# Performance work log

Hardware: AMD Instinct MI355X
Metric: run time of the kernel (lower is better)

## Reference

```python
import jax, jax.numpy as jnp
import numpy as np

# dipy lower-triangular channel order: [Dxx, Dxy, Dyy, Dxz, Dyz, Dzz]
_LOTRI_IDX = np.array([[0, 1, 3], [1, 2, 4], [3, 4, 5]])


def _trilinear_warp(img, ddf):
    """MONAI Warp(mode='bilinear', padding_mode='border'): sample img at voxel
    coords (index + ddf), trilinear interp, clamped to borders.
    img: (B,C,H,W,D), ddf: (B,3,H,W,D) in voxel units."""
    B, C, H, W, D = img.shape
    f = img.dtype
    gx, gy, gz = jnp.meshgrid(jnp.arange(H, dtype=f), jnp.arange(W, dtype=f),
                              jnp.arange(D, dtype=f), indexing='ij')
    cx = jnp.clip(gx[None] + ddf[:, 0], 0.0, H - 1.0)
    cy = jnp.clip(gy[None] + ddf[:, 1], 0.0, W - 1.0)
    cz = jnp.clip(gz[None] + ddf[:, 2], 0.0, D - 1.0)
    x0f = jnp.floor(cx); y0f = jnp.floor(cy); z0f = jnp.floor(cz)
    fx = (cx - x0f)[:, None]; fy = (cy - y0f)[:, None]; fz = (cz - z0f)[:, None]
    x0 = x0f.astype(jnp.int32); y0 = y0f.astype(jnp.int32); z0 = z0f.astype(jnp.int32)
    x1 = jnp.minimum(x0 + 1, H - 1); y1 = jnp.minimum(y0 + 1, W - 1); z1 = jnp.minimum(z0 + 1, D - 1)
    flat = img.reshape(B, C, H * W * D)

    def g(ix, iy, iz):
        lin = (ix * W + iy) * D + iz  # (B,H,W,D)
        return jnp.take_along_axis(flat, lin.reshape(B, 1, -1), axis=2).reshape(B, C, H, W, D)

    c00 = g(x0, y0, z0) * (1 - fz) + g(x0, y0, z1) * fz
    c01 = g(x0, y1, z0) * (1 - fz) + g(x0, y1, z1) * fz
    c10 = g(x1, y0, z0) * (1 - fz) + g(x1, y0, z1) * fz
    c11 = g(x1, y1, z0) * (1 - fz) + g(x1, y1, z1) * fz
    c0 = c00 * (1 - fy) + c01 * fy
    c1 = c10 * (1 - fy) + c11 * fy
    return c0 * (1 - fx) + c1 * fx


def _jacobian(ddf):
    """J = I + d(ddf)/dx via central differences (one-sided at edges).
    Returns (B,H,W,D,3,3) with J[...,i,j] = delta_ij + d ddf_i / d x_j."""
    rows = [jnp.stack(jnp.gradient(ddf[:, i], axis=(1, 2, 3)), axis=-1) for i in range(3)]
    J = jnp.stack(rows, axis=-2)  # (B,H,W,D,3,3)
    return J + jnp.eye(3, dtype=ddf.dtype)


def _forward(dti, ddf):
    warped = _trilinear_warp(dti, ddf)                    # (B,6,H,W,D)
    wc = jnp.moveaxis(warped, 1, -1)                      # (B,H,W,D,6)
    M = wc[..., jnp.asarray(_LOTRI_IDX)]                  # (B,H,W,D,3,3) symmetric
    J = _jacobian(ddf)
    U, _, Vh = jnp.linalg.svd(J, full_matrices=False)
    R = U @ Vh                                            # polar orthogonal factor
    Dp = jnp.einsum('...ji,...jk,...kl->...il', R, M, R)  # R^T M R
    lot = jnp.stack([Dp[..., 0, 0], Dp[..., 1, 0], Dp[..., 1, 1],
                     Dp[..., 2, 0], Dp[..., 2, 1], Dp[..., 2, 2]], axis=1)
    return lot


def setup_inputs() -> dict:
    key = jax.random.key(0)
    k1, k2 = jax.random.split(key)
    B, H, W, D = 1, 128, 128, 128
    dti = jax.random.normal(k1, (B, 6, H, W, D), dtype=jnp.float32)
    ddf = jax.random.normal(k2, (B, 3, H, W, D), dtype=jnp.float32)
    return {"dti": dti, "ddf": ddf}


def reference(dti, ddf):
    return _forward(dti, ddf)
```

## Files before the change

### kernel.cpp

```cpp
#include <hip/hip_runtime.h>
#include <hip/hip_fp16.h>
#include <math.h>

#define DIM 128
#define NVOX (DIM*DIM*DIM)

typedef float vfloat4 __attribute__((ext_vector_type(4)));
typedef unsigned int vuint4 __attribute__((ext_vector_type(4)));

__global__ __launch_bounds__(256) void pack_dti_kernel(
    const float* __restrict__ dti, vuint4* __restrict__ aos)
{
    const int bid = blockIdx.x;
    const int sb = ((bid & 7) << 8) | (bid >> 3);
    const int id4 = (sb * 256 + (int)threadIdx.x) * 4;

    const vfloat4 v0 = __builtin_nontemporal_load(reinterpret_cast<const vfloat4*>(dti + 0 * NVOX + id4));
    const vfloat4 v1 = __builtin_nontemporal_load(reinterpret_cast<const vfloat4*>(dti + 1 * NVOX + id4));
    const vfloat4 v2 = __builtin_nontemporal_load(reinterpret_cast<const vfloat4*>(dti + 2 * NVOX + id4));
    const vfloat4 v3 = __builtin_nontemporal_load(reinterpret_cast<const vfloat4*>(dti + 3 * NVOX + id4));
    const vfloat4 v4 = __builtin_nontemporal_load(reinterpret_cast<const vfloat4*>(dti + 4 * NVOX + id4));
    const vfloat4 v5 = __builtin_nontemporal_load(reinterpret_cast<const vfloat4*>(dti + 5 * NVOX + id4));

    auto packone = [&](float a0, float a1, float a2, float a3, float a4,
                       float a5, int idx) {
        const __half2 h01 = __floats2half2_rn(a0, a1);
        const __half2 h23 = __floats2half2_rn(a2, a3);
        const __half2 h45 = __floats2half2_rn(a4, a5);
        vuint4 q;
        q.x = *reinterpret_cast<const unsigned int*>(&h01);
        q.y = *reinterpret_cast<const unsigned int*>(&h23);
        q.z = *reinterpret_cast<const unsigned int*>(&h45);
        q.w = 0u;
        aos[idx] = q;
    };
    packone(v0.x, v1.x, v2.x, v3.x, v4.x, v5.x, id4 + 0);
    packone(v0.y, v1.y, v2.y, v3.y, v4.y, v5.y, id4 + 1);
    packone(v0.z, v1.z, v2.z, v3.z, v4.z, v5.z, id4 + 2);
    packone(v0.w, v1.w, v2.w, v3.w, v4.w, v5.w, id4 + 3);
}

__device__ __forceinline__ bool polar_f32(const float J[9], float X[9])
{
#pragma unroll
    for (int t = 0; t < 9; ++t) X[t] = J[t];
    bool bad = false;
#pragma unroll
    for (int it = 0; it < 6; ++it) {
        float C[9];
        C[0] = X[4] * X[8] - X[5] * X[7];
        C[1] = X[5] * X[6] - X[3] * X[8];
        C[2] = X[3] * X[7] - X[4] * X[6];
        C[3] = X[2] * X[7] - X[1] * X[8];
        C[4] = X[0] * X[8] - X[2] * X[6];
        C[5] = X[1] * X[6] - X[0] * X[7];
        C[6] = X[1] * X[5] - X[2] * X[4];
        C[7] = X[2] * X[3] - X[0] * X[5];
        C[8] = X[0] * X[4] - X[1] * X[3];
        const float det = X[0] * C[0] + X[1] * C[1] + X[2] * C[2];
        float a, b;
        if (it < 3) {
            float nX = 0.0f, nC = 0.0f;
#pragma unroll
            for (int t = 0; t < 9; ++t) { nX += X[t] * X[t]; nC += C[t] * C[t]; }
            if (it == 0)
                bad = !(nX * nC < 4.0e6f * det * det);
            const float s = __builtin_amdgcn_sqrtf(nC * __builtin_amdgcn_rcpf(nX));
            const float r = __builtin_amdgcn_rsqf(s * fabsf(det));
            a = 0.5f * s * r;
            b = copysignf(0.5f * r, det);
        } else {
            a = 0.5f;
            b = 0.5f * __builtin_amdgcn_rcpf(det);
        }
#pragma unroll
        for (int t = 0; t < 9; ++t) X[t] = a * X[t] + b * C[t];
    }
    return bad;
}

__device__ __forceinline__ void polar_f64(const float J[9], float X[9])
{
    double Y[9];
#pragma unroll
    for (int t = 0; t < 9; ++t) Y[t] = (double)J[t];
    for (int it = 0; it < 20; ++it) {
        double C[9];
        C[0] = Y[4] * Y[8] - Y[5] * Y[7];
        C[1] = Y[5] * Y[6] - Y[3] * Y[8];
        C[2] = Y[3] * Y[7] - Y[4] * Y[6];
        C[3] = Y[2] * Y[7] - Y[1] * Y[8];
        C[4] = Y[0] * Y[8] - Y[2] * Y[6];
        C[5] = Y[1] * Y[6] - Y[0] * Y[7];
        C[6] = Y[1] * Y[5] - Y[2] * Y[4];
        C[7] = Y[2] * Y[3] - Y[0] * Y[5];
        C[8] = Y[0] * Y[4] - Y[1] * Y[3];
        const double det = Y[0] * C[0] + Y[1] * C[1] + Y[2] * C[2];
        if (!(fabs(det) > 1e-300)) break;
        double nX = 0.0, nC = 0.0;
#pragma unroll
        for (int t = 0; t < 9; ++t) { nX += Y[t] * Y[t]; nC += C[t] * C[t]; }
        const double g = sqrt(sqrt(nC) / (fabs(det) * sqrt(nX)));
        const double a = 0.5 * g;
        const double b = 0.5 / (g * det);
        double diff2 = 0.0, n2 = 0.0;
#pragma unroll
        for (int t = 0; t < 9; ++t) {
            const double y = a * Y[t] + b * C[t];
            const double d = y - Y[t];
            diff2 += d * d; n2 += y * y;
            Y[t] = y;
        }
        if (diff2 <= 1e-26 * n2) break;
    }
#pragma unroll
    for (int t = 0; t < 9; ++t) X[t] = (float)Y[t];
}

__global__ __launch_bounds__(256) void warp_dti_kernel(
    const vuint4* __restrict__ aos,
    const float* __restrict__ ddf,
    float* __restrict__ out)
{
    const int bid = blockIdx.x;
    const int sb = ((bid & 7) << 10) | (bid >> 3);
    const int id = sb * 256 + (int)threadIdx.x;
    const int k = id & (DIM - 1);
    const int j = (id >> 7) & (DIM - 1);
    const int i = id >> 14;

    const int im = (i > 0) ? i - 1 : 0, ip = (i < DIM - 1) ? i + 1 : DIM - 1;
    const int jm = (j > 0) ? j - 1 : 0, jp = (j < DIM - 1) ? j + 1 : DIM - 1;
    const int km = (k > 0) ? k - 1 : 0, kp = (k < DIM - 1) ? k + 1 : DIM - 1;
    const float si = (ip - im == 2) ? 0.5f : 1.0f;
    const float sj = (jp - jm == 2) ? 0.5f : 1.0f;
    const float sk = (kp - km == 2) ? 0.5f : 1.0f;

    const int l_ip = (ip << 14) | (j << 7) | k;
    const int l_im = (im << 14) | (j << 7) | k;
    const int l_jp = (i << 14) | (jp << 7) | k;
    const int l_jm = (i << 14) | (jm << 7) | k;
    const int l_kp = (i << 14) | (j << 7) | kp;
    const int l_km = (i << 14) | (j << 7) | km;

    float J[9];
    float u[3];
#pragma unroll
    for (int c = 0; c < 3; ++c) {
        const float* __restrict__ p = ddf + c * NVOX;
        u[c] = p[id];
        J[c * 3 + 0] = (p[l_ip] - p[l_im]) * si;
        J[c * 3 + 1] = (p[l_jp] - p[l_jm]) * sj;
        J[c * 3 + 2] = (p[l_kp] - p[l_km]) * sk;
        J[c * 3 + c] += 1.0f;
    }

    const float cx = fminf(fmaxf((float)i + u[0], 0.0f), (float)(DIM - 1));
    const float cy = fminf(fmaxf((float)j + u[1], 0.0f), (float)(DIM - 1));
    const float cz = fminf(fmaxf((float)k + u[2], 0.0f), (float)(DIM - 1));
    const float x0f = floorf(cx), y0f = floorf(cy), z0f = floorf(cz);
    const float fx = cx - x0f, fy = cy - y0f, fz = cz - z0f;
    const int x0 = (int)x0f, y0 = (int)y0f, z0 = (int)z0f;
    const int x1 = min(x0 + 1, DIM - 1);
    const int y1 = min(y0 + 1, DIM - 1);
    const int z1 = min(z0 + 1, DIM - 1);

    const float gx0 = 1.0f - fx, gy0 = 1.0f - fy, gz0 = 1.0f - fz;

    const int dz = z1 - z0;
    const int dy = (y1 - y0) << 7;
    const int dx = (x1 - x0) << 14;
    const int b000 = (x0 << 14) | (y0 << 7) | z0;

    float acc0 = 0.0f, acc1 = 0.0f, acc2 = 0.0f;
    float acc3 = 0.0f, acc4 = 0.0f, acc5 = 0.0f;

    auto gat = [&](int lin, float wt) {
        const vuint4 q = aos[lin];
        const unsigned int qx = q.x, qy = q.y, qz = q.z;
        const __half2 h01 = *reinterpret_cast<const __half2*>(&qx);
        const __half2 h23 = *reinterpret_cast<const __half2*>(&qy);
        const __half2 h45 = *reinterpret_cast<const __half2*>(&qz);
        acc0 = fmaf(__half2float(__low2half(h01)), wt, acc0);
        acc1 = fmaf(__half2float(__high2half(h01)), wt, acc1);
        acc2 = fmaf(__half2float(__low2half(h23)), wt, acc2);
        acc3 = fmaf(__half2float(__high2half(h23)), wt, acc3);
        acc4 = fmaf(__half2float(__low2half(h45)), wt, acc4);
        acc5 = fmaf(__half2float(__high2half(h45)), wt, acc5);
    };

    gat(b000,                gx0 * gy0 * gz0);
    gat(b000 + dz,           gx0 * gy0 * fz);
    gat(b000 + dy,           gx0 * fy * gz0);
    gat(b000 + dy + dz,      gx0 * fy * fz);
    gat(b000 + dx,           fx * gy0 * gz0);
    gat(b000 + dx + dz,      fx * gy0 * fz);
    gat(b000 + dx + dy,      fx * fy * gz0);
    gat(b000 + dx + dy + dz, fx * fy * fz);

    float X[9];
    const bool bad = polar_f32(J, X);
    if (__builtin_expect(bad, 0)) polar_f64(J, X);

    const float M00 = acc0, M01 = acc1, M11 = acc2;
    const float M02 = acc3, M12 = acc4, M22 = acc5;
    float P[9];
    P[0] = M00 * X[0] + M01 * X[3] + M02 * X[6];
    P[1] = M00 * X[1] + M01 * X[4] + M02 * X[7];
    P[2] = M00 * X[2] + M01 * X[5] + M02 * X[8];
    P[3] = M01 * X[0] + M11 * X[3] + M12 * X[6];
    P[4] = M01 * X[1] + M11 * X[4] + M12 * X[7];
    P[5] = M01 * X[2] + M11 * X[5] + M12 * X[8];
    P[6] = M02 * X[0] + M12 * X[3] + M22 * X[6];
    P[7] = M02 * X[1] + M12 * X[4] + M22 * X[7];
    P[8] = M02 * X[2] + M12 * X[5] + M22 * X[8];

    __builtin_nontemporal_store(X[0] * P[0] + X[3] * P[3] + X[6] * P[6], &out[0 * NVOX + id]);
    __builtin_nontemporal_store(X[1] * P[0] + X[4] * P[3] + X[7] * P[6], &out[1 * NVOX + id]);
    __builtin_nontemporal_store(X[1] * P[1] + X[4] * P[4] + X[7] * P[7], &out[2 * NVOX + id]);
    __builtin_nontemporal_store(X[2] * P[0] + X[5] * P[3] + X[8] * P[6], &out[3 * NVOX + id]);
    __builtin_nontemporal_store(X[2] * P[1] + X[5] * P[4] + X[8] * P[7], &out[4 * NVOX + id]);
    __builtin_nontemporal_store(X[2] * P[2] + X[5] * P[5] + X[8] * P[8], &out[5 * NVOX + id]);
}

extern "C" void kernel_launch(void* const* d_in, const int* in_sizes, int n_in,
                              void* d_out, int out_size, void* d_ws, size_t ws_size,
                              hipStream_t stream) {
    const float* dti = (const float*)d_in[0];
    const float* ddf = (const float*)d_in[1];
    float* out = (float*)d_out;
    vuint4* aos = (vuint4*)d_ws;

    hipLaunchKernelGGL(pack_dti_kernel, dim3(NVOX / 1024), dim3(256), 0, stream,
                       dti, aos);
    hipLaunchKernelGGL(warp_dti_kernel, dim3(NVOX / 256), dim3(256), 0, stream,
                       aos, ddf, out);
}
```

Baseline: 167.7 us.

## Hoist all loads ahead of polar iteration, use 12-byte gathers, cut one iteration

The warp kernel now issues all 18 stencil loads of the displacement field and all 8 trilinear gathers up front, then runs the polar decomposition while those loads are in flight. The per-voxel tensor records are read as 3-dword vectors with the same 16-byte stride, so each gather fetches 12 bytes instead of 16. The float polar Newton loop drops from 6 to 5 iterations, which reduces ALU work but may leave some voxels less converged and lowers accuracy margin. Keeping the loads in flight together raises register pressure and may reduce occupancy.

```diff
diff --git a/kernel.cpp b/kernel.cpp
--- a/kernel.cpp
+++ b/kernel.cpp
@@ -7,6 +7,8 @@
 
 typedef float vfloat4 __attribute__((ext_vector_type(4)));
 typedef unsigned int vuint4 __attribute__((ext_vector_type(4)));
+typedef unsigned int vuint3 __attribute__((ext_vector_type(3)));
+static_assert(sizeof(vuint3) == 16, "vuint3 must stride 16B over the AoS array");
 
 __global__ __launch_bounds__(256) void pack_dti_kernel(
     const float* __restrict__ dti, vuint4* __restrict__ aos)
@@ -46,7 +48,7 @@
     for (int t = 0; t < 9; ++t) X[t] = J[t];
     bool bad = false;
 #pragma unroll
-    for (int it = 0; it < 6; ++it) {
+    for (int it = 0; it < 5; ++it) {
         float C[9];
         C[0] = X[4] * X[8] - X[5] * X[7];
         C[1] = X[5] * X[6] - X[3] * X[8];
@@ -118,7 +120,7 @@
 }
 
 __global__ __launch_bounds__(256) void warp_dti_kernel(
-    const vuint4* __restrict__ aos,
+    const vuint3* __restrict__ aos,
     const float* __restrict__ ddf,
     float* __restrict__ out)
 {
@@ -129,6 +131,13 @@
     const int j = (id >> 7) & (DIM - 1);
     const int i = id >> 14;
 
+    const float* __restrict__ p0_ = ddf;
+    const float* __restrict__ p1_ = ddf + NVOX;
+    const float* __restrict__ p2_ = ddf + 2 * NVOX;
+    const float u0 = p0_[id];
+    const float u1 = p1_[id];
+    const float u2 = p2_[id];
+
     const int im = (i > 0) ? i - 1 : 0, ip = (i < DIM - 1) ? i + 1 : DIM - 1;
     const int jm = (j > 0) ? j - 1 : 0, jp = (j < DIM - 1) ? j + 1 : DIM - 1;
     const int km = (k > 0) ? k - 1 : 0, kp = (k < DIM - 1) ? k + 1 : DIM - 1;
@@ -143,21 +152,16 @@
     const int l_kp = (i << 14) | (j << 7) | kp;
     const int l_km = (i << 14) | (j << 7) | km;
 
-    float J[9];
-    float u[3];
-#pragma unroll
-    for (int c = 0; c < 3; ++c) {
-        const float* __restrict__ p = ddf + c * NVOX;
-        u[c] = p[id];
-        J[c * 3 + 0] = (p[l_ip] - p[l_im]) * si;
-        J[c * 3 + 1] = (p[l_jp] - p[l_jm]) * sj;
-        J[c * 3 + 2] = (p[l_kp] - p[l_km]) * sk;
-        J[c * 3 + c] += 1.0f;
-    }
-
-    const float cx = fminf(fmaxf((float)i + u[0], 0.0f), (float)(DIM - 1));
-    const float cy = fminf(fmaxf((float)j + u[1], 0.0f), (float)(DIM - 1));
-    const float cz = fminf(fmaxf((float)k + u[2], 0.0f), (float)(DIM - 1));
+    const float n0a = p0_[l_ip], n0b = p0_[l_im], n0c = p0_[l_jp];
+    const float n0d = p0_[l_jm], n0e = p0_[l_kp], n0f = p0_[l_km];
+    const float n1a = p1_[l_ip], n1b = p1_[l_im], n1c = p1_[l_jp];
+    const float n1d = p1_[l_jm], n1e = p1_[l_kp], n1f = p1_[l_km];
+    const float n2a = p2_[l_ip], n2b = p2_[l_im], n2c = p2_[l_jp];
+    const float n2d = p2_[l_jm], n2e = p2_[l_kp], n2f = p2_[l_km];
+
+    const float cx = fminf(fmaxf((float)i + u0, 0.0f), (float)(DIM - 1));
+    const float cy = fminf(fmaxf((float)j + u1, 0.0f), (float)(DIM - 1));
+    const float cz = fminf(fmaxf((float)k + u2, 0.0f), (float)(DIM - 1));
     const float x0f = floorf(cx), y0f = floorf(cy), z0f = floorf(cz);
     const float fx = cx - x0f, fy = cy - y0f, fz = cz - z0f;
     const int x0 = (int)x0f, y0 = (int)y0f, z0 = (int)z0f;
@@ -165,18 +169,39 @@
     const int y1 = min(y0 + 1, DIM - 1);
     const int z1 = min(z0 + 1, DIM - 1);
 
-    const float gx0 = 1.0f - fx, gy0 = 1.0f - fy, gz0 = 1.0f - fz;
-
     const int dz = z1 - z0;
     const int dy = (y1 - y0) << 7;
     const int dx = (x1 - x0) << 14;
     const int b000 = (x0 << 14) | (y0 << 7) | z0;
 
+    const vuint3 q0 = aos[b000];
+    const vuint3 q1 = aos[b000 + dz];
+    const vuint3 q2 = aos[b000 + dy];
+    const vuint3 q3 = aos[b000 + dy + dz];
+    const vuint3 q4 = aos[b000 + dx];
+    const vuint3 q5 = aos[b000 + dx + dz];
+    const vuint3 q6 = aos[b000 + dx + dy];
+    const vuint3 q7 = aos[b000 + dx + dy + dz];
+
+    float J[9];
+    J[0] = (n0a - n0b) * si + 1.0f;
+    J[1] = (n0c - n0d) * sj;
+    J[2] = (n0e - n0f) * sk;
+    J[3] = (n1a - n1b) * si;
+    J[4] = (n1c - n1d) * sj + 1.0f;
+    J[5] = (n1e - n1f) * sk;
+    J[6] = (n2a - n2b) * si;
+    J[7] = (n2c - n2d) * sj;
+    J[8] = (n2e - n2f) * sk + 1.0f;
+
+    float X[9];
+    const bool bad = polar_f32(J, X);
+
+    const float gx0 = 1.0f - fx, gy0 = 1.0f - fy, gz0 = 1.0f - fz;
     float acc0 = 0.0f, acc1 = 0.0f, acc2 = 0.0f;
     float acc3 = 0.0f, acc4 = 0.0f, acc5 = 0.0f;
 
-    auto gat = [&](int lin, float wt) {
-        const vuint4 q = aos[lin];
+    auto gat = [&](const vuint3& q, float wt) {
         const unsigned int qx = q.x, qy = q.y, qz = q.z;
         const __half2 h01 = *reinterpret_cast<const __half2*>(&qx);
         const __half2 h23 = *reinterpret_cast<const __half2*>(&qy);
@@ -189,17 +214,15 @@
         acc5 = fmaf(__half2float(__high2half(h45)), wt, acc5);
     };
 
-    gat(b000,                gx0 * gy0 * gz0);
-    gat(b000 + dz,           gx0 * gy0 * fz);
-    gat(b000 + dy,           gx0 * fy * gz0);
-    gat(b000 + dy + dz,      gx0 * fy * fz);
-    gat(b000 + dx,           fx * gy0 * gz0);
-    gat(b000 + dx + dz,      fx * gy0 * fz);
-    gat(b000 + dx + dy,      fx * fy * gz0);
-    gat(b000 + dx + dy + dz, fx * fy * fz);
-
-    float X[9];
-    const bool bad = polar_f32(J, X);
+    gat(q0, gx0 * gy0 * gz0);
+    gat(q1, gx0 * gy0 * fz);
+    gat(q2, gx0 * fy * gz0);
+    gat(q3, gx0 * fy * fz);
+    gat(q4, fx * gy0 * gz0);
+    gat(q5, fx * gy0 * fz);
+    gat(q6, fx * fy * gz0);
+    gat(q7, fx * fy * fz);
+
     if (__builtin_expect(bad, 0)) polar_f64(J, X);
 
     const float M00 = acc0, M01 = acc1, M11 = acc2;
@@ -234,5 +257,5 @@
     hipLaunchKernelGGL(pack_dti_kernel, dim3(NVOX / 1024), dim3(256), 0, stream,
                        dti, aos);
     hipLaunchKernelGGL(warp_dti_kernel, dim3(NVOX / 256), dim3(256), 0, stream,
-                       aos, ddf, out);
-}
+                       (const vuint3*)aos, ddf, out);
+}
```

After: 168.7 us. About the same (+0.6%).

## Process two voxels per thread with vectorized stencil loads and hoisted gathers

Applied to the files above, without the earlier changes.

Each thread now handles two adjacent voxels along k, loading the ddf stencil as float2 and sharing the interior k-neighbours between the two voxels. All 16 gathers are issued up front, before the polar iterations, so their latency overlaps the math. The gathers read 12-byte vuint3 instead of 16-byte vuint4, and the outputs are written as float2 stores. The float polar iteration count also drops from 6 to 5, which saves ALU work but risks accuracy if the float64 fallback test does not catch slow convergence. Register pressure rises and the grid is halved, so occupancy may fall.

```diff
diff --git a/kernel.cpp b/kernel.cpp
--- a/kernel.cpp
+++ b/kernel.cpp
@@ -6,7 +6,10 @@
 #define NVOX (DIM*DIM*DIM)
 
 typedef float vfloat4 __attribute__((ext_vector_type(4)));
+typedef float vfloat2 __attribute__((ext_vector_type(2)));
 typedef unsigned int vuint4 __attribute__((ext_vector_type(4)));
+typedef unsigned int vuint3 __attribute__((ext_vector_type(3)));
+static_assert(sizeof(vuint3) == 16, "vuint3 must stride 16B over the AoS array");
 
 __global__ __launch_bounds__(256) void pack_dti_kernel(
     const float* __restrict__ dti, vuint4* __restrict__ aos)
@@ -46,7 +49,7 @@
     for (int t = 0; t < 9; ++t) X[t] = J[t];
     bool bad = false;
 #pragma unroll
-    for (int it = 0; it < 6; ++it) {
+    for (int it = 0; it < 5; ++it) {
         float C[9];
         C[0] = X[4] * X[8] - X[5] * X[7];
         C[1] = X[5] * X[6] - X[3] * X[8];
@@ -118,109 +121,169 @@
 }
 
 __global__ __launch_bounds__(256) void warp_dti_kernel(
-    const vuint4* __restrict__ aos,
+    const vuint3* __restrict__ aos,
     const float* __restrict__ ddf,
     float* __restrict__ out)
 {
     const int bid = blockIdx.x;
-    const int sb = ((bid & 7) << 10) | (bid >> 3);
-    const int id = sb * 256 + (int)threadIdx.x;
-    const int k = id & (DIM - 1);
-    const int j = (id >> 7) & (DIM - 1);
-    const int i = id >> 14;
+    const int sb = ((bid & 7) << 9) | (bid >> 3);
+    const int p = sb * 256 + (int)threadIdx.x;
+    const int vid = p << 1;
+    const int k0 = vid & (DIM - 1);
+    const int j = (vid >> 7) & (DIM - 1);
+    const int i = vid >> 14;
+
+    const float* __restrict__ p0_ = ddf;
+    const float* __restrict__ p1_ = ddf + NVOX;
+    const float* __restrict__ p2_ = ddf + 2 * NVOX;
 
     const int im = (i > 0) ? i - 1 : 0, ip = (i < DIM - 1) ? i + 1 : DIM - 1;
     const int jm = (j > 0) ? j - 1 : 0, jp = (j < DIM - 1) ? j + 1 : DIM - 1;
-    const int km = (k > 0) ? k - 1 : 0, kp = (k < DIM - 1) ? k + 1 : DIM - 1;
     const float si = (ip - im == 2) ? 0.5f : 1.0f;
     const float sj = (jp - jm == 2) ? 0.5f : 1.0f;
-    const float sk = (kp - km == 2) ? 0.5f : 1.0f;
-
-    const int l_ip = (ip << 14) | (j << 7) | k;
-    const int l_im = (im << 14) | (j << 7) | k;
-    const int l_jp = (i << 14) | (jp << 7) | k;
-    const int l_jm = (i << 14) | (jm << 7) | k;
-    const int l_kp = (i << 14) | (j << 7) | kp;
-    const int l_km = (i << 14) | (j << 7) | km;
-
-    float J[9];
-    float u[3];
+    const int km0 = (k0 > 0) ? k0 - 1 : 0;
+    const int kp1 = (k0 + 2 < DIM) ? k0 + 2 : DIM - 1;
+    const float sk0 = (k0 > 0) ? 0.5f : 1.0f;
+    const float sk1 = (k0 + 2 < DIM) ? 0.5f : 1.0f;
+
+    const int l_ip = (ip << 14) | (j << 7) | k0;
+    const int l_im = (im << 14) | (j << 7) | k0;
+    const int l_jp = (i << 14) | (jp << 7) | k0;
+    const int l_jm = (i << 14) | (jm << 7) | k0;
+    const int l_km = (i << 14) | (j << 7) | km0;
+    const int l_kp = (i << 14) | (j << 7) | kp1;
+
+    float2 uu[3], nI[3], nIm[3], nJ[3], nJm[3];
+    float skm[3], skp[3];
 #pragma unroll
     for (int c = 0; c < 3; ++c) {
-        const float* __restrict__ p = ddf + c * NVOX;
-        u[c] = p[id];
-        J[c * 3 + 0] = (p[l_ip] - p[l_im]) * si;
-        J[c * 3 + 1] = (p[l_jp] - p[l_jm]) * sj;
-        J[c * 3 + 2] = (p[l_kp] - p[l_km]) * sk;
-        J[c * 3 + c] += 1.0f;
-    }
-
-    const float cx = fminf(fmaxf((float)i + u[0], 0.0f), (float)(DIM - 1));
-    const float cy = fminf(fmaxf((float)j + u[1], 0.0f), (float)(DIM - 1));
-    const float cz = fminf(fmaxf((float)k + u[2], 0.0f), (float)(DIM - 1));
-    const float x0f = floorf(cx), y0f = floorf(cy), z0f = floorf(cz);
-    const float fx = cx - x0f, fy = cy - y0f, fz = cz - z0f;
-    const int x0 = (int)x0f, y0 = (int)y0f, z0 = (int)z0f;
-    const int x1 = min(x0 + 1, DIM - 1);
-    const int y1 = min(y0 + 1, DIM - 1);
-    const int z1 = min(z0 + 1, DIM - 1);
-
-    const float gx0 = 1.0f - fx, gy0 = 1.0f - fy, gz0 = 1.0f - fz;
-
-    const int dz = z1 - z0;
-    const int dy = (y1 - y0) << 7;
-    const int dx = (x1 - x0) << 14;
-    const int b000 = (x0 << 14) | (y0 << 7) | z0;
-
-    float acc0 = 0.0f, acc1 = 0.0f, acc2 = 0.0f;
-    float acc3 = 0.0f, acc4 = 0.0f, acc5 = 0.0f;
-
-    auto gat = [&](int lin, float wt) {
-        const vuint4 q = aos[lin];
-        const unsigned int qx = q.x, qy = q.y, qz = q.z;
+        const float* __restrict__ pc = (c == 0) ? p0_ : (c == 1) ? p1_ : p2_;
+        uu[c]  = *reinterpret_cast<const float2*>(pc + vid);
+        nI[c]  = *reinterpret_cast<const float2*>(pc + l_ip);
+        nIm[c] = *reinterpret_cast<const float2*>(pc + l_im);
+        nJ[c]  = *reinterpret_cast<const float2*>(pc + l_jp);
+        nJm[c] = *reinterpret_cast<const float2*>(pc + l_jm);
+        skm[c] = pc[l_km];
+        skp[c] = pc[l_kp];
+    }
+
+    float J0[9], J1[9];
+#pragma unroll
+    for (int c = 0; c < 3; ++c) {
+        J0[c * 3 + 0] = (nI[c].x - nIm[c].x) * si;
+        J0[c * 3 + 1] = (nJ[c].x - nJm[c].x) * sj;
+        J0[c * 3 + 2] = (uu[c].y - skm[c]) * sk0;
+        J1[c * 3 + 0] = (nI[c].y - nIm[c].y) * si;
+        J1[c * 3 + 1] = (nJ[c].y - nJm[c].y) * sj;
+        J1[c * 3 + 2] = (skp[c] - uu[c].x) * sk1;
+    }
+    J0[0] += 1.0f; J0[4] += 1.0f; J0[8] += 1.0f;
+    J1[0] += 1.0f; J1[4] += 1.0f; J1[8] += 1.0f;
+
+    int base[2], ddx[2], ddy[2], ddz[2];
+    float wfx[2], wfy[2], wfz[2];
+#pragma unroll
+    for (int v = 0; v < 2; ++v) {
+        const float ux = (v == 0) ? uu[0].x : uu[0].y;
+        const float uy = (v == 0) ? uu[1].x : uu[1].y;
+        const float uz = (v == 0) ? uu[2].x : uu[2].y;
+        const float cx = fminf(fmaxf((float)i + ux, 0.0f), (float)(DIM - 1));
+        const float cy = fminf(fmaxf((float)j + uy, 0.0f), (float)(DIM - 1));
+        const float cz = fminf(fmaxf((float)(k0 + v) + uz, 0.0f), (float)(DIM - 1));
+        const float x0f = floorf(cx), y0f = floorf(cy), z0f = floorf(cz);
+        wfx[v] = cx - x0f; wfy[v] = cy - y0f; wfz[v] = cz - z0f;
+        const int x0 = (int)x0f, y0 = (int)y0f, z0 = (int)z0f;
+        const int x1 = min(x0 + 1, DIM - 1);
+        const int y1 = min(y0 + 1, DIM - 1);
+        const int z1 = min(z0 + 1, DIM - 1);
+        ddz[v] = z1 - z0;
+        ddy[v] = (y1 - y0) << 7;
+        ddx[v] = (x1 - x0) << 14;
+        base[v] = (x0 << 14) | (y0 << 7) | z0;
+    }
+
+    vuint3 q[2][8];
+#pragma unroll
+    for (int v = 0; v < 2; ++v) {
+        q[v][0] = aos[base[v]];
+        q[v][1] = aos[base[v] + ddz[v]];
+        q[v][2] = aos[base[v] + ddy[v]];
+        q[v][3] = aos[base[v] + ddy[v] + ddz[v]];
+        q[v][4] = aos[base[v] + ddx[v]];
+        q[v][5] = aos[base[v] + ddx[v] + ddz[v]];
+        q[v][6] = aos[base[v] + ddx[v] + ddy[v]];
+        q[v][7] = aos[base[v] + ddx[v] + ddy[v] + ddz[v]];
+    }
+
+    float X0[9], X1[9];
+    const bool bad0 = polar_f32(J0, X0);
+    const bool bad1 = polar_f32(J1, X1);
+
+    float acc[2][6];
+#pragma unroll
+    for (int v = 0; v < 2; ++v)
+#pragma unroll
+        for (int t = 0; t < 6; ++t) acc[v][t] = 0.0f;
+
+    auto gat = [&](const vuint3& qq, float wt, float* a) {
+        const unsigned int qx = qq.x, qy = qq.y, qz = qq.z;
         const __half2 h01 = *reinterpret_cast<const __half2*>(&qx);
         const __half2 h23 = *reinterpret_cast<const __half2*>(&qy);
         const __half2 h45 = *reinterpret_cast<const __half2*>(&qz);
-        acc0 = fmaf(__half2float(__low2half(h01)), wt, acc0);
-        acc1 = fmaf(__half2float(__high2half(h01)), wt, acc1);
-        acc2 = fmaf(__half2float(__low2half(h23)), wt, acc2);
-        acc3 = fmaf(__half2float(__high2half(h23)), wt, acc3);
-        acc4 = fmaf(__half2float(__low2half(h45)), wt, acc4);
-        acc5 = fmaf(__half2float(__high2half(h45)), wt, acc5);
+        a[0] = fmaf(__half2float(__low2half(h01)), wt, a[0]);
+        a[1] = fmaf(__half2float(__high2half(h01)), wt, a[1]);
+        a[2] = fmaf(__half2float(__low2half(h23)), wt, a[2]);
+        a[3] = fmaf(__half2float(__high2half(h23)), wt, a[3]);
+        a[4] = fmaf(__half2float(__low2half(h45)), wt, a[4]);
+        a[5] = fmaf(__half2float(__high2half(h45)), wt, a[5]);
     };
 
-    gat(b000,                gx0 * gy0 * gz0);
-    gat(b000 + dz,           gx0 * gy0 * fz);
-    gat(b000 + dy,           gx0 * fy * gz0);
-    gat(b000 + dy + dz,      gx0 * fy * fz);
-    gat(b000 + dx,           fx * gy0 * gz0);
-    gat(b000 + dx + dz,      fx * gy0 * fz);
-    gat(b000 + dx + dy,      fx * fy * gz0);
-    gat(b000 + dx + dy + dz, fx * fy * fz);
-
-    float X[9];
-    const bool bad = polar_f32(J, X);
-    if (__builtin_expect(bad, 0)) polar_f64(J, X);
-
-    const float M00 = acc0, M01 = acc1, M11 = acc2;
-    const float M02 = acc3, M12 = acc4, M22 = acc5;
-    float P[9];
-    P[0] = M00 * X[0] + M01 * X[3] + M02 * X[6];
-    P[1] = M00 * X[1] + M01 * X[4] + M02 * X[7];
-    P[2] = M00 * X[2] + M01 * X[5] + M02 * X[8];
-    P[3] = M01 * X[0] + M11 * X[3] + M12 * X[6];
-    P[4] = M01 * X[1] + M11 * X[4] + M12 * X[7];
-    P[5] = M01 * X[2] + M11 * X[5] + M12 * X[8];
-    P[6] = M02 * X[0] + M12 * X[3] + M22 * X[6];
-    P[7] = M02 * X[1] + M12 * X[4] + M22 * X[7];
-    P[8] = M02 * X[2] + M12 * X[5] + M22 * X[8];
-
-    __builtin_nontemporal_store(X[0] * P[0] + X[3] * P[3] + X[6] * P[6], &out[0 * NVOX + id]);
-    __builtin_nontemporal_store(X[1] * P[0] + X[4] * P[3] + X[7] * P[6], &out[1 * NVOX + id]);
-    __builtin_nontemporal_store(X[1] * P[1] + X[4] * P[4] + X[7] * P[7], &out[2 * NVOX + id]);
-    __builtin_nontemporal_store(X[2] * P[0] + X[5] * P[3] + X[8] * P[6], &out[3 * NVOX + id]);
-    __builtin_nontemporal_store(X[2] * P[1] + X[5] * P[4] + X[8] * P[7], &out[4 * NVOX + id]);
-    __builtin_nontemporal_store(X[2] * P[2] + X[5] * P[5] + X[8] * P[8], &out[5 * NVOX + id]);
+#pragma unroll
+    for (int v = 0; v < 2; ++v) {
+        const float fx = wfx[v], fy = wfy[v], fz = wfz[v];
+        const float gx0 = 1.0f - fx, gy0 = 1.0f - fy, gz0 = 1.0f - fz;
+        gat(q[v][0], gx0 * gy0 * gz0, acc[v]);
+        gat(q[v][1], gx0 * gy0 * fz,  acc[v]);
+        gat(q[v][2], gx0 * fy * gz0,  acc[v]);
+        gat(q[v][3], gx0 * fy * fz,   acc[v]);
+        gat(q[v][4], fx * gy0 * gz0,  acc[v]);
+        gat(q[v][5], fx * gy0 * fz,   acc[v]);
+        gat(q[v][6], fx * fy * gz0,   acc[v]);
+        gat(q[v][7], fx * fy * fz,    acc[v]);
+    }
+
+    if (__builtin_expect(bad0, 0)) polar_f64(J0, X0);
+    if (__builtin_expect(bad1, 0)) polar_f64(J1, X1);
+
+    float o[2][6];
+#pragma unroll
+    for (int v = 0; v < 2; ++v) {
+        const float* X = (v == 0) ? X0 : X1;
+        const float M00 = acc[v][0], M01 = acc[v][1], M11 = acc[v][2];
+        const float M02 = acc[v][3], M12 = acc[v][4], M22 = acc[v][5];
+        float P[9];
+        P[0] = M00 * X[0] + M01 * X[3] + M02 * X[6];
+        P[1] = M00 * X[1] + M01 * X[4] + M02 * X[7];
+        P[2] = M00 * X[2] + M01 * X[5] + M02 * X[8];
+        P[3] = M01 * X[0] + M11 * X[3] + M12 * X[6];
+        P[4] = M01 * X[1] + M11 * X[4] + M12 * X[7];
+        P[5] = M01 * X[2] + M11 * X[5] + M12 * X[8];
+        P[6] = M02 * X[0] + M12 * X[3] + M22 * X[6];
+        P[7] = M02 * X[1] + M12 * X[4] + M22 * X[7];
+        P[8] = M02 * X[2] + M12 * X[5] + M22 * X[8];
+        o[v][0] = X[0] * P[0] + X[3] * P[3] + X[6] * P[6];
+        o[v][1] = X[1] * P[0] + X[4] * P[3] + X[7] * P[6];
+        o[v][2] = X[1] * P[1] + X[4] * P[4] + X[7] * P[7];
+        o[v][3] = X[2] * P[0] + X[5] * P[3] + X[8] * P[6];
+        o[v][4] = X[2] * P[1] + X[5] * P[4] + X[8] * P[7];
+        o[v][5] = X[2] * P[2] + X[5] * P[5] + X[8] * P[8];
+    }
+
+#pragma unroll
+    for (int t = 0; t < 6; ++t) {
+        vfloat2 w; w.x = o[0][t]; w.y = o[1][t];
+        __builtin_nontemporal_store(w, reinterpret_cast<vfloat2*>(out + t * NVOX + vid));
+    }
 }
 
 extern "C" void kernel_launch(void* const* d_in, const int* in_sizes, int n_in,
@@ -233,6 +296,6 @@
 
     hipLaunchKernelGGL(pack_dti_kernel, dim3(NVOX / 1024), dim3(256), 0, stream,
                        dti, aos);
-    hipLaunchKernelGGL(warp_dti_kernel, dim3(NVOX / 256), dim3(256), 0, stream,
-                       aos, ddf, out);
-}
+    hipLaunchKernelGGL(warp_dti_kernel, dim3(NVOX / 512), dim3(256), 0, stream,
+                       (const vuint3*)aos, ddf, out);
+}
```

New measurement: 175.3 us. 4.5% more time.

## Stage 16^3 halo tile of packed DTI in LDS for trilinear gathers

Applied to the files above, without the earlier changes.

The warp kernel becomes 8x8x8 voxel tiles with 512 threads per block. Each block first loads a 16^3 region of the packed half-precision tensor, with a 4-voxel halo, into shared memory and then does the trilinear gathers from LDS. If a displaced sample falls outside the tile it falls back to global gathers. The pack now writes 12-byte payloads into 16-byte slots, and the float32 polar iteration count drops from 6 to 5. Given the unit-variance displacements most samples should land in the tile, but each block now preloads 4096 slots (8x its voxel count) and uses 48KB of LDS, which can limit occupancy. The shorter polar iteration may also change accuracy.

```diff
diff --git a/kernel.cpp b/kernel.cpp
--- a/kernel.cpp
+++ b/kernel.cpp
@@ -5,11 +5,18 @@
 #define DIM 128
 #define NVOX (DIM*DIM*DIM)
 
+#define TILE 8
+#define PAD 4
+#define SREG 16
+#define NSLOT (SREG*SREG*SREG)
+
 typedef float vfloat4 __attribute__((ext_vector_type(4)));
 typedef unsigned int vuint4 __attribute__((ext_vector_type(4)));
+typedef unsigned int vuint3 __attribute__((ext_vector_type(3)));
+static_assert(sizeof(vuint3) == 16, "vuint3 stride assumption");
 
 __global__ __launch_bounds__(256) void pack_dti_kernel(
-    const float* __restrict__ dti, vuint4* __restrict__ aos)
+    const float* __restrict__ dti, unsigned int* __restrict__ aos)
 {
     const int bid = blockIdx.x;
     const int sb = ((bid & 7) << 8) | (bid >> 3);
@@ -27,12 +34,11 @@
         const __half2 h01 = __floats2half2_rn(a0, a1);
         const __half2 h23 = __floats2half2_rn(a2, a3);
         const __half2 h45 = __floats2half2_rn(a4, a5);
-        vuint4 q;
+        vuint3 q;
         q.x = *reinterpret_cast<const unsigned int*>(&h01);
         q.y = *reinterpret_cast<const unsigned int*>(&h23);
         q.z = *reinterpret_cast<const unsigned int*>(&h45);
-        q.w = 0u;
-        aos[idx] = q;
+        *reinterpret_cast<vuint3*>(aos + 4 * idx) = q;
     };
     packone(v0.x, v1.x, v2.x, v3.x, v4.x, v5.x, id4 + 0);
     packone(v0.y, v1.y, v2.y, v3.y, v4.y, v5.y, id4 + 1);
@@ -46,7 +52,7 @@
     for (int t = 0; t < 9; ++t) X[t] = J[t];
     bool bad = false;
 #pragma unroll
-    for (int it = 0; it < 6; ++it) {
+    for (int it = 0; it < 5; ++it) {
         float C[9];
         C[0] = X[4] * X[8] - X[5] * X[7];
         C[1] = X[5] * X[6] - X[3] * X[8];
@@ -117,17 +123,40 @@
     for (int t = 0; t < 9; ++t) X[t] = (float)Y[t];
 }
 
-__global__ __launch_bounds__(256) void warp_dti_kernel(
-    const vuint4* __restrict__ aos,
+__global__ __launch_bounds__(512) void warp_dti_kernel(
+    const unsigned int* __restrict__ aos,
     const float* __restrict__ ddf,
     float* __restrict__ out)
 {
+    __shared__ unsigned int sm[NSLOT * 3];
+
     const int bid = blockIdx.x;
-    const int sb = ((bid & 7) << 10) | (bid >> 3);
-    const int id = sb * 256 + (int)threadIdx.x;
-    const int k = id & (DIM - 1);
-    const int j = (id >> 7) & (DIM - 1);
-    const int i = id >> 14;
+    const int sb = ((bid & 7) << 9) | (bid >> 3);
+    const int tx = sb >> 8, ty = (sb >> 4) & 15, tz = sb & 15;
+    const int bx = tx << 3, by = ty << 3, bz = tz << 3;
+    const int t = (int)threadIdx.x;
+
+#pragma unroll
+    for (int r = 0; r < 8; ++r) {
+        const int s = t + (r << 9);
+        const int lx = s >> 8, ly = (s >> 4) & 15, lz = s & 15;
+        const int gx = min(max(bx - PAD + lx, 0), DIM - 1);
+        const int gy = min(max(by - PAD + ly, 0), DIM - 1);
+        const int gz = min(max(bz - PAD + lz, 0), DIM - 1);
+        const unsigned int* gp = aos + (((gx << 14) | (gy << 7) | gz) << 2);
+        const vuint3 q = *reinterpret_cast<const vuint3*>(gp);
+        const int o = s * 3;
+        sm[o + 0] = q.x; sm[o + 1] = q.y; sm[o + 2] = q.z;
+    }
+    __syncthreads();
+
+    const int vx = t >> 6, vy = (t >> 3) & 7, vz = t & 7;
+    const int i = bx + vx, j = by + vy, k = bz + vz;
+    const int id = (i << 14) | (j << 7) | k;
+
+    const float* __restrict__ p0_ = ddf;
+    const float* __restrict__ p1_ = ddf + NVOX;
+    const float* __restrict__ p2_ = ddf + 2 * NVOX;
 
     const int im = (i > 0) ? i - 1 : 0, ip = (i < DIM - 1) ? i + 1 : DIM - 1;
     const int jm = (j > 0) ? j - 1 : 0, jp = (j < DIM - 1) ? j + 1 : DIM - 1;
@@ -147,7 +176,7 @@
     float u[3];
 #pragma unroll
     for (int c = 0; c < 3; ++c) {
-        const float* __restrict__ p = ddf + c * NVOX;
+        const float* __restrict__ p = (c == 0) ? p0_ : (c == 1) ? p1_ : p2_;
         u[c] = p[id];
         J[c * 3 + 0] = (p[l_ip] - p[l_im]) * si;
         J[c * 3 + 1] = (p[l_jp] - p[l_jm]) * sj;
@@ -165,22 +194,56 @@
     const int y1 = min(y0 + 1, DIM - 1);
     const int z1 = min(z0 + 1, DIM - 1);
 
+    const int lx0 = x0 - bx + PAD, ly0 = y0 - by + PAD, lz0 = z0 - bz + PAD;
+    const int lx1 = x1 - bx + PAD, ly1 = y1 - by + PAD, lz1 = z1 - bz + PAD;
+    const bool intile =
+        ((unsigned)(lx0 | ly0 | lz0 | lx1 | ly1 | lz1) < (unsigned)SREG);
+
+    unsigned int w0[3], w1[3], w2[3], w3[3], w4[3], w5[3], w6[3], w7[3];
+    if (__builtin_expect(intile, 1)) {
+        const int l000 = (lx0 << 8) | (ly0 << 4) | lz0;
+        const int ldz = lz1 - lz0;
+        const int ldy = (ly1 - ly0) << 4;
+        const int ldx = (lx1 - lx0) << 8;
+        auto lds3 = [&](int lin, unsigned int* d) {
+            const int o = lin * 3;
+            d[0] = sm[o]; d[1] = sm[o + 1]; d[2] = sm[o + 2];
+        };
+        lds3(l000,                   w0);
+        lds3(l000 + ldz,             w1);
+        lds3(l000 + ldy,             w2);
+        lds3(l000 + ldy + ldz,       w3);
+        lds3(l000 + ldx,             w4);
+        lds3(l000 + ldx + ldz,       w5);
+        lds3(l000 + ldx + ldy,       w6);
+        lds3(l000 + ldx + ldy + ldz, w7);
+    } else {
+        const int dz = z1 - z0;
+        const int dy = (y1 - y0) << 7;
+        const int dx = (x1 - x0) << 14;
+        const int b000 = (x0 << 14) | (y0 << 7) | z0;
+        auto glb3 = [&](int lin, unsigned int* d) {
+            const unsigned int* gp = aos + (lin << 2);
+            const vuint3 q = *reinterpret_cast<const vuint3*>(gp);
+            d[0] = q.x; d[1] = q.y; d[2] = q.z;
+        };
+        glb3(b000,                w0);
+        glb3(b000 + dz,           w1);
+        glb3(b000 + dy,           w2);
+        glb3(b000 + dy + dz,      w3);
+        glb3(b000 + dx,           w4);
+        glb3(b000 + dx + dz,      w5);
+        glb3(b000 + dx + dy,      w6);
+        glb3(b000 + dx + dy + dz, w7);
+    }
+
     const float gx0 = 1.0f - fx, gy0 = 1.0f - fy, gz0 = 1.0f - fz;
-
-    const int dz = z1 - z0;
-    const int dy = (y1 - y0) << 7;
-    const int dx = (x1 - x0) << 14;
-    const int b000 = (x0 << 14) | (y0 << 7) | z0;
-
     float acc0 = 0.0f, acc1 = 0.0f, acc2 = 0.0f;
     float acc3 = 0.0f, acc4 = 0.0f, acc5 = 0.0f;
-
-    auto gat = [&](int lin, float wt) {
-        const vuint4 q = aos[lin];
-        const unsigned int qx = q.x, qy = q.y, qz = q.z;
-        const __half2 h01 = *reinterpret_cast<const __half2*>(&qx);
-        const __half2 h23 = *reinterpret_cast<const __half2*>(&qy);
-        const __half2 h45 = *reinterpret_cast<const __half2*>(&qz);
+    auto gat = [&](const unsigned int* d, float wt) {
+        const __half2 h01 = *reinterpret_cast<const __half2*>(&d[0]);
+        const __half2 h23 = *reinterpret_cast<const __half2*>(&d[1]);
+        const __half2 h45 = *reinterpret_cast<const __half2*>(&d[2]);
         acc0 = fmaf(__half2float(__low2half(h01)), wt, acc0);
         acc1 = fmaf(__half2float(__high2half(h01)), wt, acc1);
         acc2 = fmaf(__half2float(__low2half(h23)), wt, acc2);
@@ -188,15 +251,14 @@
         acc4 = fmaf(__half2float(__low2half(h45)), wt, acc4);
         acc5 = fmaf(__half2float(__high2half(h45)), wt, acc5);
     };
-
-    gat(b000,                gx0 * gy0 * gz0);
-    gat(b000 + dz,           gx0 * gy0 * fz);
-    gat(b000 + dy,           gx0 * fy * gz0);
-    gat(b000 + dy + dz,      gx0 * fy * fz);
-    gat(b000 + dx,           fx * gy0 * gz0);
-    gat(b000 + dx + dz,      fx * gy0 * fz);
-    gat(b000 + dx + dy,      fx * fy * gz0);
-    gat(b000 + dx + dy + dz, fx * fy * fz);
+    gat(w0, gx0 * gy0 * gz0);
+    gat(w1, gx0 * gy0 * fz);
+    gat(w2, gx0 * fy * gz0);
+    gat(w3, gx0 * fy * fz);
+    gat(w4, fx * gy0 * gz0);
+    gat(w5, fx * gy0 * fz);
+    gat(w6, fx * fy * gz0);
+    gat(w7, fx * fy * fz);
 
     float X[9];
     const bool bad = polar_f32(J, X);
@@ -229,10 +291,10 @@
     const float* dti = (const float*)d_in[0];
     const float* ddf = (const float*)d_in[1];
     float* out = (float*)d_out;
-    vuint4* aos = (vuint4*)d_ws;
+    unsigned int* aos = (unsigned int*)d_ws;
 
     hipLaunchKernelGGL(pack_dti_kernel, dim3(NVOX / 1024), dim3(256), 0, stream,
                        dti, aos);
-    hipLaunchKernelGGL(warp_dti_kernel, dim3(NVOX / 256), dim3(256), 0, stream,
+    hipLaunchKernelGGL(warp_dti_kernel, dim3(NVOX / 512), dim3(512), 0, stream,
                        aos, ddf, out);
 }
```

After: 197.6 us. +17.8%, slower.
